# Performance work log

Hardware: AMD Instinct MI355X
Metric: run time of the kernel (lower is better)

Reference implementation:

```python
import jax, jax.numpy as jnp
import numpy as np

WS = 7          # window size
SHIFT = 3       # shift size = ws // 2
HEADS = 16
N = WS * WS     # tokens per window


def _rel_pos_index(ws):
    coords = np.stack(np.meshgrid(np.arange(ws), np.arange(ws), indexing='ij')).reshape(2, -1)
    rel = (coords[:, :, None] - coords[:, None, :]).transpose(1, 2, 0)
    rel[:, :, 0] += ws - 1
    rel[:, :, 1] += ws - 1
    rel[:, :, 0] *= 2 * ws - 1
    return rel.sum(-1)  # [N, N] int


def _attn_mask(H, W, ws, s):
    # Swin cyclic-shift mask: windows spanning the wrap boundary get -100 on
    # cross-region pairs so softmax zeroes them out.
    img = np.zeros((H, W), np.float32)
    cnt = 0
    for hs in (slice(0, -ws), slice(-ws, -s), slice(-s, None)):
        for wsl in (slice(0, -ws), slice(-ws, -s), slice(-s, None)):
            img[hs, wsl] = cnt
            cnt += 1
    mw = img.reshape(H // ws, ws, W // ws, ws).transpose(0, 2, 1, 3).reshape(-1, ws * ws)
    diff = mw[:, None, :] - mw[:, :, None]
    return np.where(diff != 0, np.float32(-100.0), np.float32(0.0))  # [nW, N, N]


def _window_partition(x, ws):
    B, H, W, C = x.shape
    x = x.reshape(B, H // ws, ws, W // ws, ws, C).transpose(0, 1, 3, 2, 4, 5)
    return x.reshape(-1, ws * ws, C)  # [B*nW, N, C]


def _window_reverse(x, ws, B, H, W):
    C = x.shape[-1]
    x = x.reshape(B, H // ws, W // ws, ws, ws, C).transpose(0, 1, 3, 2, 4, 5)
    return x.reshape(B, H, W, C)


def setup_inputs() -> dict:
    key = jax.random.key(0)
    ks = jax.random.split(key, 5)
    B, H, W, C = 16, 56, 56, 512
    x = jax.random.normal(ks[0], (B, H, W, C), jnp.float32)
    qkv_w = jax.random.normal(ks[1], (C, 3 * C), jnp.float32) * 0.02
    qkv_b = jnp.zeros((3 * C,), jnp.float32)
    proj_w = jax.random.normal(ks[2], (C, C), jnp.float32) * 0.02
    proj_b = jnp.zeros((C,), jnp.float32)
    rel_bias_table = jax.random.normal(ks[3], ((2 * WS - 1) ** 2, HEADS), jnp.float32) * 0.02
    return {"x": x, "qkv_w": qkv_w, "qkv_b": qkv_b,
            "proj_w": proj_w, "proj_b": proj_b, "rel_bias_table": rel_bias_table}


def reference(x, qkv_w, qkv_b, proj_w, proj_b, rel_bias_table):
    B, H, W, C = x.shape
    d = C // HEADS
    scale = jnp.float32(d) ** -0.5

    rel_idx = jnp.asarray(_rel_pos_index(WS))                 # [N, N]
    mask = jnp.asarray(_attn_mask(H, W, WS, SHIFT))           # [nW, N, N]
    nW = mask.shape[0]

    shortcut = x
    # cyclic shift
    xs = jnp.roll(x, shift=(-SHIFT, -SHIFT), axis=(1, 2))
    xw = _window_partition(xs, WS)                            # [B*nW, N, C]

    qkv = xw @ qkv_w + qkv_b                                  # [B*nW, N, 3C]
    qkv = qkv.reshape(-1, N, 3, HEADS, d).transpose(2, 0, 3, 1, 4)
    q, k, v = qkv[0], qkv[1], qkv[2]                          # each [B*nW, h, N, d]

    attn = jnp.einsum('whnd,whmd->whnm', q * scale, k)        # [B*nW, h, N, N]
    # gathered relative-position bias [h, N, N]
    bias = rel_bias_table[rel_idx.reshape(-1)].reshape(N, N, HEADS).transpose(2, 0, 1)
    attn = attn + bias[None]
    # shift mask, broadcast per window
    attn = attn.reshape(B, nW, HEADS, N, N) + mask[None, :, None]
    attn = jax.nn.softmax(attn.reshape(-1, HEADS, N, N), axis=-1)

    out = jnp.einsum('whnm,whmd->whnd', attn, v)              # [B*nW, h, N, d]
    out = out.transpose(0, 2, 1, 3).reshape(-1, N, C)
    out = out @ proj_w + proj_b

    out = _window_reverse(out, WS, B, H, W)
    out = jnp.roll(out, shift=(SHIFT, SHIFT), axis=(1, 2))
    return shortcut + out
```

## Files before the change

kernel.cpp:

```cpp
#include <hip/hip_runtime.h>
#include <stdint.h>

typedef unsigned short u16;
typedef unsigned int   u32;

typedef __bf16 bf16x8 __attribute__((ext_vector_type(8)));
typedef float  f32x4  __attribute__((ext_vector_type(4)));

__device__ __forceinline__ float bf2f(u16 h) {
    return __uint_as_float(((u32)h) << 16);
}
__device__ __forceinline__ u16 f2bf(float f) {
    u32 u = __float_as_uint(f);
    u += 0x7FFFu + ((u >> 16) & 1u);
    return (u16)(u >> 16);
}

#define GLOAD_LDS16(g, l)                                                     \
    __builtin_amdgcn_global_load_lds(                                         \
        (const __attribute__((address_space(1))) void*)(g),                   \
        (__attribute__((address_space(3))) void*)(l), 16, 0, 0)

__global__ __launch_bounds__(256) void cvt_f32_bf16(const float* __restrict__ in,
                                                    u16* __restrict__ out) {
    int i = blockIdx.x * 256 + threadIdx.x;
    const float4* p = (const float4*)in + (size_t)i * 2;
    float4 a = p[0], b = p[1];
    union { u16 s[8]; uint4 v; } o;
    o.s[0] = f2bf(a.x); o.s[1] = f2bf(a.y); o.s[2] = f2bf(a.z); o.s[3] = f2bf(a.w);
    o.s[4] = f2bf(b.x); o.s[5] = f2bf(b.y); o.s[6] = f2bf(b.z); o.s[7] = f2bf(b.w);
    ((uint4*)out)[i] = o.v;
}

__global__ void transpose_cvt(const float* __restrict__ in, u16* __restrict__ out,
                              int R, int Cc) {
    __shared__ float tile[32][33];
    int c0 = blockIdx.x * 32, r0 = blockIdx.y * 32;
    int tx = threadIdx.x, ty = threadIdx.y;
    tile[ty][tx] = in[(size_t)(r0 + ty) * Cc + c0 + tx];
    __syncthreads();
    out[(size_t)(c0 + ty) * R + r0 + tx] = f2bf(tile[tx][ty]);
}

__global__ __launch_bounds__(64) void build_bias(const float* __restrict__ table,
                                                 float* __restrict__ biasL) {
    int cls = blockIdx.x >> 4;
    int h   = blockIdx.x & 15;
    int lane = threadIdx.x;
    int quad = lane >> 4, l16 = lane & 15;
    int eh = cls >> 1, ew = cls & 1;
    float* base = biasL + (size_t)(cls * 16 + h) * 4096;
#pragma unroll
    for (int mi = 0; mi < 4; mi++) {
#pragma unroll
        for (int ni = 0; ni < 4; ni++) {
            float4 v;
            float* vp = &v.x;
#pragma unroll
            for (int r = 0; r < 4; r++) {
                int m = mi * 16 + quad * 4 + r;
                int c = ni * 16 + l16;
                float b;
                if (c >= 49)      b = -1e9f;
                else if (m >= 49) b = 0.f;
                else {
                    int ty = m / 7, tx = m % 7, jy = c / 7, jx = c % 7;
                    b = table[((ty - jy + 6) * 13 + (tx - jx + 6)) * 16 + h];
                    int ridr = (eh ? (ty < 4 ? 1 : 2) : 0) * 3 + (ew ? (tx < 4 ? 1 : 2) : 0);
                    int ridc = (eh ? (jy < 4 ? 1 : 2) : 0) * 3 + (ew ? (jx < 4 ? 1 : 2) : 0);
                    if (ridr != ridc) b -= 100.f;
                }
                vp[r] = b;
            }
            ((float4*)base)[((mi * 4 + ni) * 4 + quad) * 16 + l16] = v;
        }
    }
}

template <bool OUT_F32>
__global__ __launch_bounds__(512, 2) void gemm256(
    const u16* __restrict__ A, const u16* __restrict__ Bt,
    const float* __restrict__ bias, const float* __restrict__ res,
    void* __restrict__ Cout, int M, int N, int K, int GX)
{
    __shared__ __align__(16) char smem[131072];
    char* AsB = smem;
    char* BsB = smem + 65536;

    const int nwg = (int)gridDim.x;
    int wg = (int)blockIdx.x;
    wg = (wg & 7) * (nwg >> 3) + (wg >> 3);
    const int bx = wg % GX;
    const int by = wg / GX;
    const size_t m0 = (size_t)by * 256;
    const size_t n0 = (size_t)bx * 256;

    const int t    = threadIdx.x;
    const int lane = t & 63;
    const int w    = t >> 6;
    const int wm   = w >> 2, wn = w & 3;
    const int quad = lane >> 4, l16 = lane & 15;
    const int xr   = l16 & 7;
    const int cb   = (quad ^ xr) * 16;

    const int r0  = t >> 3;
    const int s8  = t & 7;
    const int swz = (s8 ^ (r0 & 7)) * 8;
    const u16* Ag0 = A  + (m0 + r0) * K + swz;
    const u16* Bg0 = Bt + (n0 + r0) * K + swz;
    const size_t j64K = (size_t)64 * K;
    const int lo0 = t * 16, lo1 = t * 16 + 8192;

    auto stageA = [&](int bf, int half, int ktt) {
        char* d = AsB + bf * 32768 + half * 16384;
        const u16* g = Ag0 + (size_t)half * 128 * K + ktt * 64;
        GLOAD_LDS16(g, d + lo0);
        GLOAD_LDS16(g + j64K, d + lo1);
    };
    auto stageB = [&](int bf, int half, int ktt) {
        char* d = BsB + bf * 32768 + half * 16384;
        const u16* g = Bg0 + (size_t)half * 128 * K + ktt * 64;
        GLOAD_LDS16(g, d + lo0);
        GLOAD_LDS16(g + j64K, d + lo1);
    };

    f32x4 acc[8][4];
    const f32x4 fz = {0.f, 0.f, 0.f, 0.f};
#pragma unroll
    for (int i = 0; i < 8; i++)
#pragma unroll
        for (int j = 0; j < 4; j++) acc[i][j] = fz;

    const int NT = K >> 6;

    stageA(0, 0, 0); stageA(0, 1, 0); stageB(0, 0, 0); stageB(0, 1, 0);
    stageB(1, 0, 1); stageA(1, 0, 1);
    asm volatile("s_waitcnt vmcnt(4)" ::: "memory");
    __builtin_amdgcn_s_barrier();

    for (int kt = 0; kt < NT; ++kt) {
        const int buf = kt & 1;
        const char* Ab  = AsB + buf * 32768 + wm * 16384 + l16 * 128;
        const char* Bb  = BsB + buf * 32768 + (wn >> 1) * 16384 + (wn & 1) * 8192 + l16 * 128;
        const char* pA0 = Ab + cb;
        const char* pA1 = Ab + (cb ^ 64);
        const char* pB0 = Bb + cb;
        const char* pB1 = Bb + (cb ^ 64);

        bf16x8 a[4][2], b0[2][2], b1[2][2];

#pragma unroll
        for (int mi = 0; mi < 4; mi++) {
            a[mi][0] = *(const bf16x8*)(pA0 + mi * 2048);
            a[mi][1] = *(const bf16x8*)(pA1 + mi * 2048);
        }
#pragma unroll
        for (int nj = 0; nj < 2; nj++) {
            b0[nj][0] = *(const bf16x8*)(pB0 + nj * 2048);
            b0[nj][1] = *(const bf16x8*)(pB1 + nj * 2048);
        }
        if (kt + 1 < NT) stageA((kt + 1) & 1, 1, kt + 1);
        __builtin_amdgcn_s_barrier();
        asm volatile("s_waitcnt lgkmcnt(0)" ::: "memory");
        __builtin_amdgcn_s_setprio(1);
#pragma unroll
        for (int mi = 0; mi < 4; mi++)
#pragma unroll
            for (int nj = 0; nj < 2; nj++) {
                acc[mi][nj] = __builtin_amdgcn_mfma_f32_16x16x32_bf16(
                    a[mi][0], b0[nj][0], acc[mi][nj], 0, 0, 0);
                acc[mi][nj] = __builtin_amdgcn_mfma_f32_16x16x32_bf16(
                    a[mi][1], b0[nj][1], acc[mi][nj], 0, 0, 0);
            }
        __builtin_amdgcn_s_setprio(0);
        __builtin_amdgcn_s_barrier();

#pragma unroll
        for (int nj = 0; nj < 2; nj++) {
            b1[nj][0] = *(const bf16x8*)(pB0 + 4096 + nj * 2048);
            b1[nj][1] = *(const bf16x8*)(pB1 + 4096 + nj * 2048);
        }
        if (kt + 1 < NT) stageB((kt + 1) & 1, 1, kt + 1);
        __builtin_amdgcn_s_barrier();
        asm volatile("s_waitcnt lgkmcnt(0)" ::: "memory");
        __builtin_amdgcn_s_setprio(1);
#pragma unroll
        for (int mi = 0; mi < 4; mi++)
#pragma unroll
            for (int nj = 0; nj < 2; nj++) {
                acc[mi][2 + nj] = __builtin_amdgcn_mfma_f32_16x16x32_bf16(
                    a[mi][0], b1[nj][0], acc[mi][2 + nj], 0, 0, 0);
                acc[mi][2 + nj] = __builtin_amdgcn_mfma_f32_16x16x32_bf16(
                    a[mi][1], b1[nj][1], acc[mi][2 + nj], 0, 0, 0);
            }
        __builtin_amdgcn_s_setprio(0);
        __builtin_amdgcn_s_barrier();

#pragma unroll
        for (int mi = 0; mi < 4; mi++) {
            a[mi][0] = *(const bf16x8*)(pA0 + 8192 + mi * 2048);
            a[mi][1] = *(const bf16x8*)(pA1 + 8192 + mi * 2048);
        }
        if (kt + 2 < NT) stageB(buf, 0, kt + 2);
        __builtin_amdgcn_s_barrier();
        asm volatile("s_waitcnt lgkmcnt(0)" ::: "memory");
        __builtin_amdgcn_s_setprio(1);
#pragma unroll
        for (int mi = 0; mi < 4; mi++)
#pragma unroll
            for (int nj = 0; nj < 2; nj++) {
                acc[4 + mi][2 + nj] = __builtin_amdgcn_mfma_f32_16x16x32_bf16(
                    a[mi][0], b1[nj][0], acc[4 + mi][2 + nj], 0, 0, 0);
                acc[4 + mi][2 + nj] = __builtin_amdgcn_mfma_f32_16x16x32_bf16(
                    a[mi][1], b1[nj][1], acc[4 + mi][2 + nj], 0, 0, 0);
            }
        __builtin_amdgcn_s_setprio(0);
        __builtin_amdgcn_s_barrier();

        if (kt + 2 < NT) stageA(buf, 0, kt + 2);
        __builtin_amdgcn_s_barrier();
        __builtin_amdgcn_s_setprio(1);
#pragma unroll
        for (int mi = 0; mi < 4; mi++)
#pragma unroll
            for (int nj = 0; nj < 2; nj++) {
                acc[4 + mi][nj] = __builtin_amdgcn_mfma_f32_16x16x32_bf16(
                    a[mi][0], b0[nj][0], acc[4 + mi][nj], 0, 0, 0);
                acc[4 + mi][nj] = __builtin_amdgcn_mfma_f32_16x16x32_bf16(
                    a[mi][1], b0[nj][1], acc[4 + mi][nj], 0, 0, 0);
            }
        __builtin_amdgcn_s_setprio(0);
        if (kt < NT - 2) asm volatile("s_waitcnt vmcnt(4)" ::: "memory");
        else             asm volatile("s_waitcnt vmcnt(0)" ::: "memory");
        __builtin_amdgcn_s_barrier();
    }

    float* scr = (float*)(void*)smem + w * 1088;
    float bv[4];
#pragma unroll
    for (int nj = 0; nj < 4; nj++)
        bv[nj] = bias[n0 + wn * 64 + nj * 16 + l16];

    const size_t colb = n0 + wn * 64 + quad * 16;
#pragma unroll
    for (int mi = 0; mi < 8; mi++) {
#pragma unroll
        for (int nj = 0; nj < 4; nj++)
#pragma unroll
            for (int r = 0; r < 4; r++)
                scr[(quad * 4 + r) * 68 + nj * 16 + l16] = acc[mi][nj][r] + bv[nj];
        __builtin_amdgcn_s_waitcnt(0);

        const size_t row = m0 + wm * 128 + mi * 16 + l16;
        const float4* sp = (const float4*)(scr + l16 * 68 + quad * 16);
        float4 v0 = sp[0], v1 = sp[1], v2 = sp[2], v3 = sp[3];

        if (OUT_F32) {
            const float4* rp = (const float4*)(res + row * N + colb);
            float4 r0v = rp[0], r1v = rp[1], r2v = rp[2], r3v = rp[3];
            v0.x += r0v.x; v0.y += r0v.y; v0.z += r0v.z; v0.w += r0v.w;
            v1.x += r1v.x; v1.y += r1v.y; v1.z += r1v.z; v1.w += r1v.w;
            v2.x += r2v.x; v2.y += r2v.y; v2.z += r2v.z; v2.w += r2v.w;
            v3.x += r3v.x; v3.y += r3v.y; v3.z += r3v.z; v3.w += r3v.w;
            float4* op = (float4*)((float*)Cout + row * N + colb);
            op[0] = v0; op[1] = v1; op[2] = v2; op[3] = v3;
        } else {
            union { u16 s[8]; uint4 q; } p0, p1;
            p0.s[0] = f2bf(v0.x); p0.s[1] = f2bf(v0.y); p0.s[2] = f2bf(v0.z); p0.s[3] = f2bf(v0.w);
            p0.s[4] = f2bf(v1.x); p0.s[5] = f2bf(v1.y); p0.s[6] = f2bf(v1.z); p0.s[7] = f2bf(v1.w);
            p1.s[0] = f2bf(v2.x); p1.s[1] = f2bf(v2.y); p1.s[2] = f2bf(v2.z); p1.s[3] = f2bf(v2.w);
            p1.s[4] = f2bf(v3.x); p1.s[5] = f2bf(v3.y); p1.s[6] = f2bf(v3.z); p1.s[7] = f2bf(v3.w);
            uint4* op = (uint4*)((u16*)Cout + row * N + colb);
            op[0] = p0.q; op[1] = p1.q;
        }
        __builtin_amdgcn_s_waitcnt(0);
    }
}

__global__ __launch_bounds__(64) void attn_kernel(
    const u16* __restrict__ qkv, const float* __restrict__ biasL,
    u16* __restrict__ O)
{
    __shared__ __align__(16) u16 Ps[64 * 72];
    __shared__ __align__(16) u16 Vts[32 * 72];

    const int wid = blockIdx.x >> 4;
    const int h   = blockIdx.x & 15;
    const int b   = wid >> 6;
    const int wy  = (wid >> 3) & 7;
    const int wx  = wid & 7;
    const int cls = ((wy == 7) ? 2 : 0) + ((wx == 7) ? 1 : 0);
    const int lane = threadIdx.x;
    const int quad = lane >> 4, l16 = lane & 15;

    auto tokOf = [&](int m) -> size_t {
        int tt = m < 49 ? m : 48;
        int ty = tt / 7, tx = tt - ty * 7;
        int ho = wy * 7 + ty + 3; if (ho >= 56) ho -= 56;
        int wo = wx * 7 + tx + 3; if (wo >= 56) wo -= 56;
        return ((size_t)b * 56 + ho) * 56 + wo;
    };

    {
        size_t tok = tokOf(lane);
        const uint4* vs = (const uint4*)(qkv + tok * 1536 + 1024 + h * 32);
        union { uint4 u4[4]; u16 s[32]; } vb;
        vb.u4[0] = vs[0]; vb.u4[1] = vs[1]; vb.u4[2] = vs[2]; vb.u4[3] = vs[3];
#pragma unroll
        for (int d = 0; d < 32; d++) Vts[d * 72 + lane] = vb.s[d];
    }

    bf16x8 aq[4], bk[4];
#pragma unroll
    for (int i = 0; i < 4; i++) {
        size_t tok = tokOf(i * 16 + l16);
        const u16* base = qkv + tok * 1536 + h * 32 + quad * 8;
        aq[i] = *(const bf16x8*)base;
        bk[i] = *(const bf16x8*)(base + 512);
    }

    f32x4 acc[4][4];
    {
        const f32x4 fzz = {0.f, 0.f, 0.f, 0.f};
#pragma unroll
        for (int mi = 0; mi < 4; mi++)
#pragma unroll
            for (int ni = 0; ni < 4; ni++)
                acc[mi][ni] = __builtin_amdgcn_mfma_f32_16x16x32_bf16(
                    aq[mi], bk[ni], fzz, 0, 0, 0);
    }

    {
        const float scale = 0.17677669529663687f;
        const float* bp = biasL + (size_t)(cls * 16 + h) * 4096;
#pragma unroll
        for (int mi = 0; mi < 4; mi++)
#pragma unroll
            for (int ni = 0; ni < 4; ni++) {
                float4 bvv = ((const float4*)bp)[((mi * 4 + ni) * 4 + quad) * 16 + l16];
                const float* bvp = &bvv.x;
#pragma unroll
                for (int r = 0; r < 4; r++)
                    acc[mi][ni][r] = acc[mi][ni][r] * scale + bvp[r];
            }
    }

    float rinv[4][4];
    {
#pragma unroll
        for (int mi = 0; mi < 4; mi++)
#pragma unroll
            for (int r = 0; r < 4; r++) {
                float m0 = fmaxf(fmaxf(acc[mi][0][r], acc[mi][1][r]),
                                 fmaxf(acc[mi][2][r], acc[mi][3][r]));
                m0 = fmaxf(m0, __shfl_xor(m0, 1, 64));
                m0 = fmaxf(m0, __shfl_xor(m0, 2, 64));
                m0 = fmaxf(m0, __shfl_xor(m0, 4, 64));
                m0 = fmaxf(m0, __shfl_xor(m0, 8, 64));
                float e0 = __expf(acc[mi][0][r] - m0);
                float e1 = __expf(acc[mi][1][r] - m0);
                float e2 = __expf(acc[mi][2][r] - m0);
                float e3 = __expf(acc[mi][3][r] - m0);
                acc[mi][0][r] = e0; acc[mi][1][r] = e1;
                acc[mi][2][r] = e2; acc[mi][3][r] = e3;
                float s0 = (e0 + e1) + (e2 + e3);
                s0 += __shfl_xor(s0, 1, 64);
                s0 += __shfl_xor(s0, 2, 64);
                s0 += __shfl_xor(s0, 4, 64);
                s0 += __shfl_xor(s0, 8, 64);
                rinv[mi][r] = __builtin_amdgcn_rcpf(s0);
            }
    }

#pragma unroll
    for (int mi = 0; mi < 4; mi++)
#pragma unroll
        for (int ni = 0; ni < 4; ni++)
#pragma unroll
            for (int r = 0; r < 4; r++)
                Ps[(mi * 16 + quad * 4 + r) * 72 + ni * 16 + l16] =
                    f2bf(acc[mi][ni][r]);
    __syncthreads();

#pragma unroll
    for (int mi = 0; mi < 4; mi++) {
        f32x4 c0 = {0.f, 0.f, 0.f, 0.f}, c1 = {0.f, 0.f, 0.f, 0.f};
#pragma unroll
        for (int ks = 0; ks < 2; ks++) {
            bf16x8 a = *(const bf16x8*)(Ps + (mi * 16 + l16) * 72 + ks * 32 + quad * 8);
            bf16x8 b0 = *(const bf16x8*)(Vts + l16 * 72 + ks * 32 + quad * 8);
            bf16x8 b1 = *(const bf16x8*)(Vts + (16 + l16) * 72 + ks * 32 + quad * 8);
            c0 = __builtin_amdgcn_mfma_f32_16x16x32_bf16(a, b0, c0, 0, 0, 0);
            c1 = __builtin_amdgcn_mfma_f32_16x16x32_bf16(a, b1, c1, 0, 0, 0);
        }
#pragma unroll
        for (int r = 0; r < 4; r++) {
            int m = mi * 16 + quad * 4 + r;
            if (m < 49) {
                int ty = m / 7, tx = m - ty * 7;
                int ho = wy * 7 + ty + 3; if (ho >= 56) ho -= 56;
                int wo = wx * 7 + tx + 3; if (wo >= 56) wo -= 56;
                size_t tok = ((size_t)b * 56 + ho) * 56 + wo;
                u16* op = O + tok * 512 + h * 32 + l16;
                op[0]  = f2bf(c0[r] * rinv[mi][r]);
                op[16] = f2bf(c1[r] * rinv[mi][r]);
            }
        }
    }
}

extern "C" void kernel_launch(void* const* d_in, const int* in_sizes, int n_in,
                              void* d_out, int out_size, void* d_ws, size_t ws_size,
                              hipStream_t stream)
{
    const float* x      = (const float*)d_in[0];
    const float* qkv_w  = (const float*)d_in[1];
    const float* qkv_b  = (const float*)d_in[2];
    const float* proj_w = (const float*)d_in[3];
    const float* proj_b = (const float*)d_in[4];
    const float* table  = (const float*)d_in[5];
    float* out = (float*)d_out;

    const int M  = 16 * 56 * 56;
    const int Cd = 512, C3 = 1536;

    char* ws = (char*)d_ws;
    u16* QKV  = (u16*)ws;
    u16* Xb   = (u16*)(ws + (size_t)M * C3 * 2);
    u16* Obuf = Xb;
    u16* Wt1  = (u16*)(ws + (size_t)M * C3 * 2 + (size_t)M * Cd * 2);
    u16* Wt2  = Wt1 + (size_t)C3 * Cd;
    float* biasL = (float*)Wt1;

    cvt_f32_bf16<<<(M * Cd) / 2048, 256, 0, stream>>>(x, Xb);

    dim3 tb(32, 32);
    transpose_cvt<<<dim3(C3 / 32, Cd / 32), tb, 0, stream>>>(qkv_w, Wt1, Cd, C3);
    transpose_cvt<<<dim3(Cd / 32, Cd / 32), tb, 0, stream>>>(proj_w, Wt2, Cd, Cd);

    gemm256<false><<<dim3((M / 256) * (C3 / 256)), 512, 0, stream>>>(
        Xb, Wt1, qkv_b, nullptr, QKV, M, C3, Cd, C3 / 256);

    build_bias<<<dim3(64), 64, 0, stream>>>(table, biasL);

    attn_kernel<<<dim3(1024 * 16), 64, 0, stream>>>(QKV, biasL, Obuf);

    gemm256<true><<<dim3((M / 256) * (Cd / 256)), 512, 0, stream>>>(
        Obuf, Wt2, proj_b, x, out, M, Cd, Cd, Cd / 256);
}
```

Measured before the change: 453.7 us.

## Shrink GEMM tile to 128x256 with simplified two-phase pipeline

Changes the GEMM workgroup tile from 256x256 to 128x256, halving per-wave accumulators and LDS use, and doubles the grid size. The K-loop is restructured from four MFMA phases to two, with the next tile's A halves and second B half prefetched at once. The epilogue waits only on LDS counters instead of a full waitcnt. This is meant to raise occupancy and wave count for better CU balance on the M=50176 problem, at the cost of lower arithmetic intensity per tile and more global reads of B.

```diff
diff --git a/kernel.cpp b/kernel.cpp
--- a/kernel.cpp
+++ b/kernel.cpp
@@ -78,21 +78,21 @@
 }
 
 template <bool OUT_F32>
-__global__ __launch_bounds__(512, 2) void gemm256(
+__global__ __launch_bounds__(512, 2) void gemm128(
     const u16* __restrict__ A, const u16* __restrict__ Bt,
     const float* __restrict__ bias, const float* __restrict__ res,
     void* __restrict__ Cout, int M, int N, int K, int GX)
 {
-    __shared__ __align__(16) char smem[131072];
+    __shared__ __align__(16) char smem[98304];
     char* AsB = smem;
-    char* BsB = smem + 65536;
+    char* BsB = smem + 32768;
 
     const int nwg = (int)gridDim.x;
     int wg = (int)blockIdx.x;
     wg = (wg & 7) * (nwg >> 3) + (wg >> 3);
     const int bx = wg % GX;
     const int by = wg / GX;
-    const size_t m0 = (size_t)by * 256;
+    const size_t m0 = (size_t)by * 128;
     const size_t n0 = (size_t)bx * 256;
 
     const int t    = threadIdx.x;
@@ -109,45 +109,42 @@
     const u16* Ag0 = A  + (m0 + r0) * K + swz;
     const u16* Bg0 = Bt + (n0 + r0) * K + swz;
     const size_t j64K = (size_t)64 * K;
-    const int lo0 = t * 16, lo1 = t * 16 + 8192;
 
     auto stageA = [&](int bf, int half, int ktt) {
-        char* d = AsB + bf * 32768 + half * 16384;
-        const u16* g = Ag0 + (size_t)half * 128 * K + ktt * 64;
-        GLOAD_LDS16(g, d + lo0);
-        GLOAD_LDS16(g + j64K, d + lo1);
+        char* d = AsB + bf * 16384 + half * 8192 + t * 16;
+        GLOAD_LDS16(Ag0 + (size_t)half * j64K + ktt * 64, d);
     };
     auto stageB = [&](int bf, int half, int ktt) {
         char* d = BsB + bf * 32768 + half * 16384;
         const u16* g = Bg0 + (size_t)half * 128 * K + ktt * 64;
-        GLOAD_LDS16(g, d + lo0);
-        GLOAD_LDS16(g + j64K, d + lo1);
+        GLOAD_LDS16(g, d + t * 16);
+        GLOAD_LDS16(g + j64K, d + t * 16 + 8192);
     };
 
-    f32x4 acc[8][4];
+    f32x4 acc[4][4];
     const f32x4 fz = {0.f, 0.f, 0.f, 0.f};
 #pragma unroll
-    for (int i = 0; i < 8; i++)
+    for (int i = 0; i < 4; i++)
 #pragma unroll
         for (int j = 0; j < 4; j++) acc[i][j] = fz;
 
     const int NT = K >> 6;
 
     stageA(0, 0, 0); stageA(0, 1, 0); stageB(0, 0, 0); stageB(0, 1, 0);
-    stageB(1, 0, 1); stageA(1, 0, 1);
-    asm volatile("s_waitcnt vmcnt(4)" ::: "memory");
+    stageB(1, 0, 1);
+    asm volatile("s_waitcnt vmcnt(2)" ::: "memory");
     __builtin_amdgcn_s_barrier();
 
     for (int kt = 0; kt < NT; ++kt) {
-        const int buf = kt & 1;
-        const char* Ab  = AsB + buf * 32768 + wm * 16384 + l16 * 128;
-        const char* Bb  = BsB + buf * 32768 + (wn >> 1) * 16384 + (wn & 1) * 8192 + l16 * 128;
+        const int buf = kt & 1, nb = buf ^ 1;
+        const char* Ab  = AsB + buf * 16384 + wm * 8192 + l16 * 128;
+        const char* Bb  = BsB + buf * 32768 + wn * 8192 + l16 * 128;
         const char* pA0 = Ab + cb;
         const char* pA1 = Ab + (cb ^ 64);
         const char* pB0 = Bb + cb;
         const char* pB1 = Bb + (cb ^ 64);
 
-        bf16x8 a[4][2], b0[2][2], b1[2][2];
+        bf16x8 a[4][2], b[2][2];
 
 #pragma unroll
         for (int mi = 0; mi < 4; mi++) {
@@ -156,10 +153,14 @@
         }
 #pragma unroll
         for (int nj = 0; nj < 2; nj++) {
-            b0[nj][0] = *(const bf16x8*)(pB0 + nj * 2048);
-            b0[nj][1] = *(const bf16x8*)(pB1 + nj * 2048);
-        }
-        if (kt + 1 < NT) stageA((kt + 1) & 1, 1, kt + 1);
+            b[nj][0] = *(const bf16x8*)(pB0 + nj * 2048);
+            b[nj][1] = *(const bf16x8*)(pB1 + nj * 2048);
+        }
+        if (kt + 1 < NT) {
+            stageA(nb, 0, kt + 1);
+            stageA(nb, 1, kt + 1);
+            stageB(nb, 1, kt + 1);
+        }
         __builtin_amdgcn_s_barrier();
         asm volatile("s_waitcnt lgkmcnt(0)" ::: "memory");
         __builtin_amdgcn_s_setprio(1);
@@ -168,38 +169,17 @@
 #pragma unroll
             for (int nj = 0; nj < 2; nj++) {
                 acc[mi][nj] = __builtin_amdgcn_mfma_f32_16x16x32_bf16(
-                    a[mi][0], b0[nj][0], acc[mi][nj], 0, 0, 0);
+                    a[mi][0], b[nj][0], acc[mi][nj], 0, 0, 0);
                 acc[mi][nj] = __builtin_amdgcn_mfma_f32_16x16x32_bf16(
-                    a[mi][1], b0[nj][1], acc[mi][nj], 0, 0, 0);
+                    a[mi][1], b[nj][1], acc[mi][nj], 0, 0, 0);
             }
         __builtin_amdgcn_s_setprio(0);
         __builtin_amdgcn_s_barrier();
 
 #pragma unroll
         for (int nj = 0; nj < 2; nj++) {
-            b1[nj][0] = *(const bf16x8*)(pB0 + 4096 + nj * 2048);
-            b1[nj][1] = *(const bf16x8*)(pB1 + 4096 + nj * 2048);
-        }
-        if (kt + 1 < NT) stageB((kt + 1) & 1, 1, kt + 1);
-        __builtin_amdgcn_s_barrier();
-        asm volatile("s_waitcnt lgkmcnt(0)" ::: "memory");
-        __builtin_amdgcn_s_setprio(1);
-#pragma unroll
-        for (int mi = 0; mi < 4; mi++)
-#pragma unroll
-            for (int nj = 0; nj < 2; nj++) {
-                acc[mi][2 + nj] = __builtin_amdgcn_mfma_f32_16x16x32_bf16(
-                    a[mi][0], b1[nj][0], acc[mi][2 + nj], 0, 0, 0);
-                acc[mi][2 + nj] = __builtin_amdgcn_mfma_f32_16x16x32_bf16(
-                    a[mi][1], b1[nj][1], acc[mi][2 + nj], 0, 0, 0);
-            }
-        __builtin_amdgcn_s_setprio(0);
-        __builtin_amdgcn_s_barrier();
-
-#pragma unroll
-        for (int mi = 0; mi < 4; mi++) {
-            a[mi][0] = *(const bf16x8*)(pA0 + 8192 + mi * 2048);
-            a[mi][1] = *(const bf16x8*)(pA1 + 8192 + mi * 2048);
+            b[nj][0] = *(const bf16x8*)(pB0 + 4096 + nj * 2048);
+            b[nj][1] = *(const bf16x8*)(pB1 + 4096 + nj * 2048);
         }
         if (kt + 2 < NT) stageB(buf, 0, kt + 2);
         __builtin_amdgcn_s_barrier();
@@ -209,28 +189,13 @@
         for (int mi = 0; mi < 4; mi++)
 #pragma unroll
             for (int nj = 0; nj < 2; nj++) {
-                acc[4 + mi][2 + nj] = __builtin_amdgcn_mfma_f32_16x16x32_bf16(
-                    a[mi][0], b1[nj][0], acc[4 + mi][2 + nj], 0, 0, 0);
-                acc[4 + mi][2 + nj] = __builtin_amdgcn_mfma_f32_16x16x32_bf16(
-                    a[mi][1], b1[nj][1], acc[4 + mi][2 + nj], 0, 0, 0);
+                acc[mi][2 + nj] = __builtin_amdgcn_mfma_f32_16x16x32_bf16(
+                    a[mi][0], b[nj][0], acc[mi][2 + nj], 0, 0, 0);
+                acc[mi][2 + nj] = __builtin_amdgcn_mfma_f32_16x16x32_bf16(
+                    a[mi][1], b[nj][1], acc[mi][2 + nj], 0, 0, 0);
             }
         __builtin_amdgcn_s_setprio(0);
-        __builtin_amdgcn_s_barrier();
-
-        if (kt + 2 < NT) stageA(buf, 0, kt + 2);
-        __builtin_amdgcn_s_barrier();
-        __builtin_amdgcn_s_setprio(1);
-#pragma unroll
-        for (int mi = 0; mi < 4; mi++)
-#pragma unroll
-            for (int nj = 0; nj < 2; nj++) {
-                acc[4 + mi][nj] = __builtin_amdgcn_mfma_f32_16x16x32_bf16(
-                    a[mi][0], b0[nj][0], acc[4 + mi][nj], 0, 0, 0);
-                acc[4 + mi][nj] = __builtin_amdgcn_mfma_f32_16x16x32_bf16(
-                    a[mi][1], b0[nj][1], acc[4 + mi][nj], 0, 0, 0);
-            }
-        __builtin_amdgcn_s_setprio(0);
-        if (kt < NT - 2) asm volatile("s_waitcnt vmcnt(4)" ::: "memory");
+        if (kt + 2 < NT) asm volatile("s_waitcnt vmcnt(2)" ::: "memory");
         else             asm volatile("s_waitcnt vmcnt(0)" ::: "memory");
         __builtin_amdgcn_s_barrier();
     }
@@ -243,15 +208,15 @@
 
     const size_t colb = n0 + wn * 64 + quad * 16;
 #pragma unroll
-    for (int mi = 0; mi < 8; mi++) {
+    for (int mi = 0; mi < 4; mi++) {
 #pragma unroll
         for (int nj = 0; nj < 4; nj++)
 #pragma unroll
             for (int r = 0; r < 4; r++)
                 scr[(quad * 4 + r) * 68 + nj * 16 + l16] = acc[mi][nj][r] + bv[nj];
-        __builtin_amdgcn_s_waitcnt(0);
-
-        const size_t row = m0 + wm * 128 + mi * 16 + l16;
+        asm volatile("s_waitcnt lgkmcnt(0)" ::: "memory");
+
+        const size_t row = m0 + wm * 64 + mi * 16 + l16;
         const float4* sp = (const float4*)(scr + l16 * 68 + quad * 16);
         float4 v0 = sp[0], v1 = sp[1], v2 = sp[2], v3 = sp[3];
 
@@ -273,7 +238,7 @@
             uint4* op = (uint4*)((u16*)Cout + row * N + colb);
             op[0] = p0.q; op[1] = p1.q;
         }
-        __builtin_amdgcn_s_waitcnt(0);
+        asm volatile("s_waitcnt lgkmcnt(0)" ::: "memory");
     }
 }
 
@@ -438,13 +403,13 @@
     transpose_cvt<<<dim3(C3 / 32, Cd / 32), tb, 0, stream>>>(qkv_w, Wt1, Cd, C3);
     transpose_cvt<<<dim3(Cd / 32, Cd / 32), tb, 0, stream>>>(proj_w, Wt2, Cd, Cd);
 
-    gemm256<false><<<dim3((M / 256) * (C3 / 256)), 512, 0, stream>>>(
+    gemm128<false><<<dim3((M / 128) * (C3 / 256)), 512, 0, stream>>>(
         Xb, Wt1, qkv_b, nullptr, QKV, M, C3, Cd, C3 / 256);
 
     build_bias<<<dim3(64), 64, 0, stream>>>(table, biasL);
 
     attn_kernel<<<dim3(1024 * 16), 64, 0, stream>>>(QKV, biasL, Obuf);
 
-    gemm256<true><<<dim3((M / 256) * (Cd / 256)), 512, 0, stream>>>(
+    gemm128<true><<<dim3((M / 128) * (Cd / 256)), 512, 0, stream>>>(
         Obuf, Wt2, proj_b, x, out, M, Cd, Cd, Cd / 256);
 }
```

Result: slower. 470.9 us (+3.8%).
